# Kernel tuning notes

Measured on AMD Instinct MI355X. Metric: run time of the kernel, lower is better.

## Reference

```python
import jax, jax.numpy as jnp
import numpy as np

N = 100000      # nodes
E = 1600000     # edges (before self-loops)
IN_DIM = 128
HEADS1, C1 = 8, 16   # conv1: hidden_dim=16, heads=8 -> 128 concat
OUT_DIM = 40
NEG_SLOPE = 0.2


def setup_inputs() -> dict:
    key = jax.random.key(0)
    ks = jax.random.split(key, 10)
    s = 0.1
    x = jax.random.normal(ks[0], (N, IN_DIM), dtype=jnp.float32)
    edge_index = jax.random.randint(ks[1], (2, E), 0, N)
    W1 = jax.random.normal(ks[2], (IN_DIM, HEADS1 * C1), dtype=jnp.float32) * s
    att_l1 = jax.random.normal(ks[3], (HEADS1, C1), dtype=jnp.float32) * s
    att_r1 = jax.random.normal(ks[4], (HEADS1, C1), dtype=jnp.float32) * s
    b1 = jnp.zeros((HEADS1 * C1,), dtype=jnp.float32)
    W2 = jax.random.normal(ks[5], (HEADS1 * C1, OUT_DIM), dtype=jnp.float32) * s
    att_l2 = jax.random.normal(ks[6], (1, OUT_DIM), dtype=jnp.float32) * s
    att_r2 = jax.random.normal(ks[7], (1, OUT_DIM), dtype=jnp.float32) * s
    b2 = jnp.zeros((OUT_DIM,), dtype=jnp.float32)
    return {"x": x, "edge_index": edge_index, "W1": W1, "att_l1": att_l1,
            "att_r1": att_r1, "b1": b1, "W2": W2, "att_l2": att_l2,
            "att_r2": att_r2, "b2": b2}


def supergat_layer(x, src, dst, W, att_l, att_r, bias, concat):
    """One SuperGATConv layer, MX attention, inference mode (no dropout)."""
    n = x.shape[0]
    heads, out_ch = att_l.shape
    h = (x @ W).reshape(n, heads, out_ch)      # [N, H, C]
    h_i = h[dst]                               # target features  [E2, H, C]
    h_j = h[src]                               # source features  [E2, H, C]
    # MX attention: mix of GO (learned att vectors) gated by DP (dot product)
    logits = jnp.sum(h_i * h_j, axis=-1)                           # [E2, H]
    alpha = jnp.sum(h_j * att_l, axis=-1) + jnp.sum(h_i * att_r, axis=-1)
    alpha = alpha * jax.nn.sigmoid(logits)
    alpha = jax.nn.leaky_relu(alpha, NEG_SLOPE)
    # segment softmax over destination node (every node has a self-loop)
    a_max = jax.ops.segment_max(alpha, dst, num_segments=n)        # [N, H]
    ex = jnp.exp(alpha - a_max[dst])
    denom = jax.ops.segment_sum(ex, dst, num_segments=n)           # [N, H]
    a = ex / denom[dst]                                            # [E2, H]
    out = jax.ops.segment_sum(h_j * a[..., None], dst, num_segments=n)  # [N,H,C]
    if concat:
        out = out.reshape(n, heads * out_ch)
    else:
        out = out.mean(axis=1)
    return out + bias


def reference(x, edge_index, W1, att_l1, att_r1, b1, W2, att_l2, att_r2, b2):
    n = x.shape[0]
    loops = jnp.arange(n, dtype=edge_index.dtype)
    ei = jnp.concatenate([edge_index, jnp.stack([loops, loops])], axis=1)
    src, dst = ei[0], ei[1]
    h = supergat_layer(x, src, dst, W1, att_l1, att_r1, b1, concat=True)
    h = jax.nn.elu(h)
    out = supergat_layer(h, src, dst, W2, att_l2, att_r2, b2, concat=False)
    return jax.nn.log_softmax(out, axis=1)
```

## Files before the change

kernel.cpp:

```cpp
#include <hip/hip_runtime.h>
#include <math.h>

#define N_NODES 100000
#define N_EDGES 1600000
#define E2 (N_EDGES + N_NODES)
#define NEG_SLOPE 0.2f

#define NPB 128
#define NB  ((N_NODES + NPB - 1) / NPB)
#define CAP 2600
#define CAPP (CAP + 3 * NPB)
#define BSLACK (3 * NPB + 4)
#define BCH 4096

typedef unsigned int uint;
typedef unsigned short ushort;
typedef __attribute__((ext_vector_type(2))) _Float16 h2_t;
typedef __attribute__((ext_vector_type(8))) _Float16 f16x8;
typedef __attribute__((ext_vector_type(4))) float f32x4;

union U8 { uint4 q; f16x8 v; h2_t h2[4]; _Float16 h[8]; uint u[4]; };


__device__ inline ushort f2h(float x) {
  _Float16 h = (_Float16)x;
  return *(ushort*)&h;
}

__device__ inline float h2f(ushort u) {
  _Float16 h = *(_Float16*)&u;
  return (float)h;
}

__device__ inline h2_t pk2h(float a, float b) {
  auto r = __builtin_amdgcn_cvt_pkrtz(a, b);
  return *(h2_t*)&r;
}

__device__ inline float fdot2(h2_t a, h2_t b, float c) {
#if __has_builtin(__builtin_amdgcn_fdot2)
  return __builtin_amdgcn_fdot2(*(__fp16 __attribute__((ext_vector_type(2)))*)&a,
                                *(__fp16 __attribute__((ext_vector_type(2)))*)&b,
                                c, false);
#else
  return c + (float)a.x * (float)b.x + (float)a.y * (float)b.y;
#endif
}


__global__ __launch_bounds__(256) void k_prepW(const float* __restrict__ W1,
                                               const float* __restrict__ W2,
                                               ushort* __restrict__ WT1,
                                               ushort* __restrict__ WT2,
                                               int* __restrict__ bcursor) {
  int b = blockIdx.x, t = threadIdx.x;
  if (b == 0) {
    for (int i = t; i < 128 * 128; i += 256) {
      int k = i >> 7, n = i & 127;
      WT1[n * 128 + k] = f2h(W1[i]);
    }
  } else if (b == 1) {
    for (int i = t; i < 48 * 128; i += 256) {
      int n = i >> 7, k = i & 127;
      WT2[i] = (n < 40) ? f2h(W2[k * 40 + n]) : (ushort)0;
    }
  } else {
    for (int i = t; i < NB; i += 256) bcursor[i] = i * CAP;
  }
}


__global__ __launch_bounds__(256) void k_bucket(const int* __restrict__ ei,
                                                int* __restrict__ bcursor,
                                                uint* __restrict__ pbuf) {
  __shared__ uint pay[BCH];
  __shared__ ushort bkt[BCH];
  __shared__ int cnt[NB];
  __shared__ int base[NB];
  const int tid = threadIdx.x;
  const int ebase = blockIdx.x * BCH;
  for (int t = tid; t < NB; t += 256) cnt[t] = 0;
  __syncthreads();
#pragma unroll 4
  for (int k = 0; k < BCH / 256; ++k) {
    int idx = tid + k * 256;
    int e = ebase + idx;
    if (e < E2) {
      int s, d;
      if (e < N_EDGES) { s = ei[e]; d = ei[N_EDGES + e]; }
      else { s = e - N_EDGES; d = s; }
      pay[idx] = ((uint)s << 7) | (uint)(d & 127);
      int b = d >> 7;
      bkt[idx] = (ushort)b;
      atomicAdd(&cnt[b], 1);
    } else {
      bkt[idx] = 0xFFFFu;
    }
  }
  __syncthreads();
  for (int t = tid; t < NB; t += 256) {
    int c = cnt[t];
    base[t] = c ? atomicAdd(&bcursor[t], c) : 0;
    cnt[t] = 0;
  }
  __syncthreads();
#pragma unroll 4
  for (int k = 0; k < BCH / 256; ++k) {
    int idx = tid + k * 256;
    ushort b = bkt[idx];
    if (b != 0xFFFFu) {
      int pos = base[b] + atomicAdd(&cnt[b], 1);
      pbuf[pos] = pay[idx];
    }
  }
}

__global__ __launch_bounds__(1024) void k_scanB(const int* __restrict__ bcursor,
                                                int* __restrict__ bbase) {
  __shared__ int sm[1024];
  int t = threadIdx.x;
  int v = (t < NB) ? (bcursor[t] - t * CAP) : 0;
  sm[t] = v;
  __syncthreads();
  for (int off = 1; off < 1024; off <<= 1) {
    int u = (t >= off) ? sm[t - off] : 0;
    __syncthreads();
    sm[t] += u;
    __syncthreads();
  }
  if (t < NB) {
    int excl = sm[t] - v;
    bbase[t] = ((excl + 3) & ~3) + t * BSLACK;
  }
}

__global__ __launch_bounds__(128) void k_csr(const uint* __restrict__ pbuf,
                                             const int* __restrict__ bcursor,
                                             const int* __restrict__ bbase,
                                             int* __restrict__ rs,
                                             int* __restrict__ re,
                                             int* __restrict__ csr) {
  __shared__ int hist[NPB];
  __shared__ int excl[NPB];
  __shared__ int cur[NPB];
  __shared__ int lcsr[CAPP];
  const int b = blockIdx.x;
  const int tid = threadIdx.x;
  int count = bcursor[b] - b * CAP;
  if (count > CAP) count = CAP;
  const int gbase = bbase[b];
  const uint* seg = pbuf + b * CAP;
  hist[tid] = 0;
  __syncthreads();
  for (int k = tid; k < count; k += 128) atomicAdd(&hist[seg[k] & 127u], 1);
  __syncthreads();
  int rounded = (hist[tid] + 3) & ~3;
  excl[tid] = rounded;
  __syncthreads();
  for (int off = 1; off < 128; off <<= 1) {
    int u = (tid >= off) ? excl[tid - off] : 0;
    __syncthreads();
    excl[tid] += u;
    __syncthreads();
  }
  int ex = excl[tid] - rounded;
  cur[tid] = ex;
  int node = b * NPB + tid;
  if (node < N_NODES) {
    rs[node] = gbase + ex;
    re[node] = gbase + ex + rounded;
  }
  __syncthreads();
  const int ptotal = excl[NPB - 1];
  for (int k = tid; k < ptotal; k += 128) lcsr[k] = N_NODES;
  __syncthreads();
  for (int k = tid; k < count; k += 128) {
    uint pk = seg[k];
    int nd = pk & 127u;
    int pos = atomicAdd(&cur[nd], 1);
    lcsr[pos] = (int)(pk >> 7);
  }
  __syncthreads();
  for (int k = tid; k < ptotal; k += 128) csr[gbase + k] = lcsr[k];
}


__global__ __launch_bounds__(256) void k_gemm1m(const float* __restrict__ x,
                                                const ushort* __restrict__ WT1,
                                                const float* __restrict__ attl,
                                                const float* __restrict__ attr,
                                                ushort* __restrict__ h1h,
                                                ushort* __restrict__ al1h,
                                                float* __restrict__ ar1) {
  __shared__ ushort stg[4][16][136];
  __shared__ h2_t attl_sm[64], attr_sm[64];
  const int tid = threadIdx.x;
  const int w = tid >> 6, l = tid & 63;
  const int r16 = l & 15, kq = l >> 4;
  const int rowbase = blockIdx.x * 64 + w * 16;
  if (tid < 64) attl_sm[tid] = pk2h(attl[2 * tid], attl[2 * tid + 1]);
  else if (tid < 128) { int t = tid - 64; attr_sm[t] = pk2h(attr[2 * t], attr[2 * t + 1]); }
  if (blockIdx.x == 0) {
    if (tid >= 128 && tid < 144) ((uint4*)h1h)[(size_t)N_NODES * 16 + (tid - 128)] = make_uint4(0, 0, 0, 0);
    else if (tid >= 144 && tid < 152) al1h[(size_t)N_NODES * 8 + (tid - 144)] = (ushort)0xFC00;
  }
  int arow = rowbase + r16;
  if (arow > N_NODES - 1) arow = N_NODES - 1;
  f16x8 af[4];
  const float* xr = x + (size_t)arow * 128 + kq * 8;
#pragma unroll
  for (int t = 0; t < 4; ++t) {
    float4 a0 = *(const float4*)(xr + t * 32);
    float4 a1 = *(const float4*)(xr + t * 32 + 4);
    U8 u;
    u.h2[0] = pk2h(a0.x, a0.y); u.h2[1] = pk2h(a0.z, a0.w);
    u.h2[2] = pk2h(a1.x, a1.y); u.h2[3] = pk2h(a1.z, a1.w);
    af[t] = u.v;
  }
  f32x4 acc[8];
#pragma unroll
  for (int n = 0; n < 8; ++n) acc[n] = (f32x4){0.f, 0.f, 0.f, 0.f};
  const uint4* WT4 = (const uint4*)WT1;
#pragma unroll
  for (int t = 0; t < 4; ++t) {
#pragma unroll
    for (int n = 0; n < 8; ++n) {
      U8 b;
      b.q = WT4[(size_t)(n * 16 + r16) * 16 + t * 4 + kq];
      acc[n] = __builtin_amdgcn_mfma_f32_16x16x32_f16(af[t], b.v, acc[n], 0, 0, 0);
    }
  }
#pragma unroll
  for (int n = 0; n < 8; ++n) {
#pragma unroll
    for (int r = 0; r < 4; ++r) stg[w][kq * 4 + r][n * 16 + r16] = f2h(acc[n][r]);
  }
  __syncthreads();
  uint4* H1 = (uint4*)h1h;
  const uint4* S = (const uint4*)stg[w];
#pragma unroll
  for (int q = 0; q < 4; ++q) {
    int idx = l + q * 64;
    int row = idx >> 4, c4 = idx & 15;
    int grow = rowbase + row;
    if (grow < N_NODES) H1[(size_t)grow * 16 + c4] = S[row * 17 + c4];
  }
#pragma unroll
  for (int p = 0; p < 2; ++p) {
    int pidx = l + p * 64;
    int row = pidx >> 3, h = pidx & 7;
    int grow = rowbase + row;
    U8 a0, a1;
    a0.q = S[row * 17 + h * 2];
    a1.q = S[row * 17 + h * 2 + 1];
    float sl = 0.f, sr = 0.f;
#pragma unroll
    for (int k = 0; k < 4; ++k) {
      sl = fdot2(a0.h2[k], attl_sm[h * 8 + k], sl);
      sr = fdot2(a0.h2[k], attr_sm[h * 8 + k], sr);
      sl = fdot2(a1.h2[k], attl_sm[h * 8 + 4 + k], sl);
      sr = fdot2(a1.h2[k], attr_sm[h * 8 + 4 + k], sr);
    }
    if (grow < N_NODES) {
      al1h[(size_t)grow * 8 + h] = f2h(sl);
      ar1[(size_t)grow * 8 + h] = sr;
    }
  }
}


__global__ __launch_bounds__(256) void k_edge1(const ushort* __restrict__ h1h,
                                               const ushort* __restrict__ alT,
                                               const float* __restrict__ ar1,
                                               const int* __restrict__ rs,
                                               const int* __restrict__ re,
                                               const int* __restrict__ csr,
                                               const float* __restrict__ b1,
                                               ushort* __restrict__ y1h) {
  const int tid = threadIdx.x;
  const int lane = tid & 63;
  const int wv = tid >> 6;
  const int grp = lane >> 4;
  const int l = lane & 15;
  const int h = l >> 1;
  const int node0 = (blockIdx.x * 4 + wv) * 4 + grp;
  const bool alive = node0 < N_NODES;
  const int i = alive ? node0 : N_NODES - 1;
  const int start = rs[i], end = re[i];
  const char* Hb = (const char*)h1h;
  const char* Ab = (const char*)alT;
  const char* Cb = (const char*)csr;
  const uint loff = (uint)l * 16u;
  const uint aoff = (uint)h * 2u;
  U8 uhi;
  uhi.q = *(const uint4*)(Hb + (uint)i * 256u + loff);
  const float ar_i = ar1[i * 8 + h];
  float s = 0.f;
  f16x8 acc = {};
  int4 ja = *(const int4*)(Cb + (uint)start * 4u);
  for (int e = start; e < end; e += 4) {
    int ep = (e + 4 < end) ? e + 4 : e;
    int4 jn = *(const int4*)(Cb + (uint)ep * 4u);
    U8 u0, u1, u2, u3;
    u0.q = *(const uint4*)(Hb + (uint)ja.x * 256u + loff);
    u1.q = *(const uint4*)(Hb + (uint)ja.y * 256u + loff);
    u2.q = *(const uint4*)(Hb + (uint)ja.z * 256u + loff);
    u3.q = *(const uint4*)(Hb + (uint)ja.w * 256u + loff);
    float av0 = h2f(*(const ushort*)(Ab + (uint)ja.x * 16u + aoff));
    float av1 = h2f(*(const ushort*)(Ab + (uint)ja.y * 16u + aoff));
    float av2 = h2f(*(const ushort*)(Ab + (uint)ja.z * 16u + aoff));
    float av3 = h2f(*(const ushort*)(Ab + (uint)ja.w * 16u + aoff));
    float p0 = 0.f, p1 = 0.f, p2 = 0.f, p3 = 0.f;
#pragma unroll
    for (int k = 0; k < 4; ++k) {
      p0 = fdot2(uhi.h2[k], u0.h2[k], p0);
      p1 = fdot2(uhi.h2[k], u1.h2[k], p1);
      p2 = fdot2(uhi.h2[k], u2.h2[k], p2);
      p3 = fdot2(uhi.h2[k], u3.h2[k], p3);
    }
    p0 += __shfl_xor(p0, 1);
    p1 += __shfl_xor(p1, 1);
    p2 += __shfl_xor(p2, 1);
    p3 += __shfl_xor(p3, 1);
    float a0 = (av0 + ar_i) * (1.f / (1.f + __expf(-p0)));
    float a1 = (av1 + ar_i) * (1.f / (1.f + __expf(-p1)));
    float a2 = (av2 + ar_i) * (1.f / (1.f + __expf(-p2)));
    float a3 = (av3 + ar_i) * (1.f / (1.f + __expf(-p3)));
    a0 = fmaxf(a0, NEG_SLOPE * a0);
    a1 = fmaxf(a1, NEG_SLOPE * a1);
    a2 = fmaxf(a2, NEG_SLOPE * a2);
    a3 = fmaxf(a3, NEG_SLOPE * a3);
    float ex0 = __expf(a0);
    float ex1 = __expf(a1);
    float ex2 = __expf(a2);
    float ex3 = __expf(a3);
    s += (ex0 + ex1) + (ex2 + ex3);
    acc += u0.v * (_Float16)ex0;
    acc += u1.v * (_Float16)ex1;
    acc += u2.v * (_Float16)ex2;
    acc += u3.v * (_Float16)ex3;
    ja = jn;
  }
  float inv = 1.f / s;
  float4 bb0 = *(const float4*)(b1 + l * 8);
  float4 bb1 = *(const float4*)(b1 + l * 8 + 4);
  float o[8];
#pragma unroll
  for (int c = 0; c < 8; ++c) {
    float b = (c < 4) ? ((const float*)&bb0)[c] : ((const float*)&bb1)[c - 4];
    float v = (float)acc[c] * inv + b;
    o[c] = v > 0.f ? v : __expf(v) - 1.f;
  }
  if (alive) {
    U8 pk;
#pragma unroll
    for (int c = 0; c < 4; ++c) pk.h2[c] = pk2h(o[2 * c], o[2 * c + 1]);
    ((uint4*)y1h)[(size_t)i * 16 + l] = pk.q;
  }
}


__global__ __launch_bounds__(256) void k_gemm2m(const ushort* __restrict__ y1h,
                                                const ushort* __restrict__ WT2,
                                                const float* __restrict__ attl,
                                                const float* __restrict__ attr,
                                                ushort* __restrict__ h2p,
                                                float* __restrict__ al2,
                                                float* __restrict__ ar2) {
  __shared__ ushort stg[4][16][56];
  __shared__ h2_t attl_sm[20], attr_sm[20];
  const int tid = threadIdx.x;
  const int w = tid >> 6, l = tid & 63;
  const int r16 = l & 15, kq = l >> 4;
  const int rowbase = blockIdx.x * 64 + w * 16;
  if (tid < 20) attl_sm[tid] = pk2h(attl[2 * tid], attl[2 * tid + 1]);
  else if (tid >= 32 && tid < 52) { int t = tid - 32; attr_sm[t] = pk2h(attr[2 * t], attr[2 * t + 1]); }
  if (blockIdx.x == 0) {
    if (tid >= 64 && tid < 69) ((uint4*)h2p)[(size_t)N_NODES * 5 + (tid - 64)] = make_uint4(0, 0, 0, 0);
    else if (tid == 69) al2[N_NODES] = -INFINITY;
  }
  int arow = rowbase + r16;
  if (arow > N_NODES - 1) arow = N_NODES - 1;
  const uint4* Y4 = (const uint4*)y1h;
  f16x8 af[4];
#pragma unroll
  for (int t = 0; t < 4; ++t) {
    U8 u;
    u.q = Y4[(size_t)arow * 16 + t * 4 + kq];
    af[t] = u.v;
  }
  f32x4 acc[3];
#pragma unroll
  for (int n = 0; n < 3; ++n) acc[n] = (f32x4){0.f, 0.f, 0.f, 0.f};
  const uint4* WT4 = (const uint4*)WT2;
#pragma unroll
  for (int t = 0; t < 4; ++t) {
#pragma unroll
    for (int n = 0; n < 3; ++n) {
      U8 b;
      b.q = WT4[(size_t)(n * 16 + r16) * 16 + t * 4 + kq];
      acc[n] = __builtin_amdgcn_mfma_f32_16x16x32_f16(af[t], b.v, acc[n], 0, 0, 0);
    }
  }
#pragma unroll
  for (int n = 0; n < 3; ++n) {
#pragma unroll
    for (int r = 0; r < 4; ++r) stg[w][kq * 4 + r][n * 16 + r16] = f2h(acc[n][r]);
  }
  __syncthreads();
  uint4* H2 = (uint4*)h2p;
  const uint4* S = (const uint4*)stg[w];
#pragma unroll
  for (int q = 0; q < 2; ++q) {
    int idx = l + q * 64;
    if (idx < 80) {
      int row = idx / 5, c4 = idx % 5;
      int grow = rowbase + row;
      if (grow < N_NODES) H2[(size_t)grow * 5 + c4] = S[row * 7 + c4];
    }
  }
  if (l < 32) {
    int row = l & 15, sel = l >> 4;
    int grow = rowbase + row;
    const h2_t* att = sel ? attr_sm : attl_sm;
    float v = 0.f;
#pragma unroll
    for (int q = 0; q < 5; ++q) {
      U8 b;
      b.q = S[row * 7 + q];
#pragma unroll
      for (int k = 0; k < 4; ++k) v = fdot2(b.h2[k], att[q * 4 + k], v);
    }
    if (grow < N_NODES) {
      if (sel) ar2[grow] = v;
      else     al2[grow] = v;
    }
  }
}


__global__ __launch_bounds__(256) void k_edge2(const ushort* __restrict__ h2p,
                                               const float* __restrict__ alT,
                                               const float* __restrict__ ar2,
                                               const int* __restrict__ rs,
                                               const int* __restrict__ re,
                                               const int* __restrict__ csr,
                                               const float* __restrict__ b2,
                                               float* __restrict__ out) {
  const int tid = threadIdx.x;
  const int lane = tid & 63;
  const int wv = tid >> 6;
  const int grp = lane >> 3;
  const int l = lane & 7;
  const int node0 = (blockIdx.x * 4 + wv) * 8 + grp;
  const bool alive = node0 < N_NODES;
  const int i = alive ? node0 : N_NODES - 1;
  const int start = rs[i], end = re[i];
  const char* Hb = (const char*)h2p;
  const char* Cb = (const char*)csr;
  const uint loff = (uint)(l < 5 ? l : 0) * 16u;
  U8 uhi;
  uhi.q = *(const uint4*)(Hb + (uint)i * 80u + loff);
  if (l >= 5) uhi.q = make_uint4(0, 0, 0, 0);
  const float ar_i = ar2[i];
  float s = 0.f;
  f16x8 acc = {};
  int4 ja = *(const int4*)(Cb + (uint)start * 4u);
  for (int e = start; e < end; e += 4) {
    int ep = (e + 4 < end) ? e + 4 : e;
    int4 jn = *(const int4*)(Cb + (uint)ep * 4u);
    U8 u0, u1, u2, u3;
    u0.q = *(const uint4*)(Hb + (uint)ja.x * 80u + loff);
    u1.q = *(const uint4*)(Hb + (uint)ja.y * 80u + loff);
    u2.q = *(const uint4*)(Hb + (uint)ja.z * 80u + loff);
    u3.q = *(const uint4*)(Hb + (uint)ja.w * 80u + loff);
    float av0 = alT[ja.x], av1 = alT[ja.y], av2 = alT[ja.z], av3 = alT[ja.w];
    float p0 = 0.f, p1 = 0.f, p2 = 0.f, p3 = 0.f;
#pragma unroll
    for (int k = 0; k < 4; ++k) {
      p0 = fdot2(uhi.h2[k], u0.h2[k], p0);
      p1 = fdot2(uhi.h2[k], u1.h2[k], p1);
      p2 = fdot2(uhi.h2[k], u2.h2[k], p2);
      p3 = fdot2(uhi.h2[k], u3.h2[k], p3);
    }
#pragma unroll
    for (int m = 1; m <= 4; m <<= 1) {
      p0 += __shfl_xor(p0, m);
      p1 += __shfl_xor(p1, m);
      p2 += __shfl_xor(p2, m);
      p3 += __shfl_xor(p3, m);
    }
    float a0 = (av0 + ar_i) * (1.f / (1.f + __expf(-p0)));
    float a1 = (av1 + ar_i) * (1.f / (1.f + __expf(-p1)));
    float a2 = (av2 + ar_i) * (1.f / (1.f + __expf(-p2)));
    float a3 = (av3 + ar_i) * (1.f / (1.f + __expf(-p3)));
    a0 = fmaxf(a0, NEG_SLOPE * a0);
    a1 = fmaxf(a1, NEG_SLOPE * a1);
    a2 = fmaxf(a2, NEG_SLOPE * a2);
    a3 = fmaxf(a3, NEG_SLOPE * a3);
    float ex0 = __expf(a0);
    float ex1 = __expf(a1);
    float ex2 = __expf(a2);
    float ex3 = __expf(a3);
    s += (ex0 + ex1) + (ex2 + ex3);
    acc += u0.v * (_Float16)ex0;
    acc += u1.v * (_Float16)ex1;
    acc += u2.v * (_Float16)ex2;
    acc += u3.v * (_Float16)ex3;
    ja = jn;
  }
  float inv = 1.f / s;
  bool act = l < 5;
  float o[8];
  float mx = -1e30f;
#pragma unroll
  for (int c = 0; c < 8; ++c) {
    float b = act ? b2[l * 8 + c] : 0.f;
    o[c] = (float)acc[c] * inv + b;
    if (act) mx = fmaxf(mx, o[c]);
  }
  mx = fmaxf(mx, __shfl_xor(mx, 1));
  mx = fmaxf(mx, __shfl_xor(mx, 2));
  mx = fmaxf(mx, __shfl_xor(mx, 4));
  float se = 0.f;
  if (act) {
#pragma unroll
    for (int c = 0; c < 8; ++c) se += __expf(o[c] - mx);
  }
  se += __shfl_xor(se, 1);
  se += __shfl_xor(se, 2);
  se += __shfl_xor(se, 4);
  if (alive && act) {
    float lse = mx + __logf(se);
    float4 r0 = make_float4(o[0] - lse, o[1] - lse, o[2] - lse, o[3] - lse);
    float4 r1 = make_float4(o[4] - lse, o[5] - lse, o[6] - lse, o[7] - lse);
    float4* O = (float4*)(out + (size_t)i * 40 + l * 8);
    O[0] = r0;
    O[1] = r1;
  }
}


extern "C" void kernel_launch(void* const* d_in, const int* in_sizes, int n_in,
                              void* d_out, int out_size, void* d_ws, size_t ws_size,
                              hipStream_t stream) {
  const float* x     = (const float*)d_in[0];
  const int*   ei    = (const int*)d_in[1];
  const float* W1    = (const float*)d_in[2];
  const float* attl1 = (const float*)d_in[3];
  const float* attr1 = (const float*)d_in[4];
  const float* b1    = (const float*)d_in[5];
  const float* W2    = (const float*)d_in[6];
  const float* attl2 = (const float*)d_in[7];
  const float* attr2 = (const float*)d_in[8];
  const float* b2    = (const float*)d_in[9];
  float* out = (float*)d_out;

  char* wsp = (char*)d_ws;
  size_t off = 0;
  auto alloc = [&](size_t bytes) {
    char* p = wsp + off;
    off = (off + bytes + 255) & ~(size_t)255;
    return p;
  };
  ushort* h1h   = (ushort*)alloc((size_t)(N_NODES + 1) * 128 * 2);
  ushort* y1h   = (ushort*)alloc((size_t)N_NODES * 128 * 2);
  ushort* al1h  = (ushort*)alloc((size_t)(N_NODES + 1) * 8 * 2);
  float* ar1    = (float*)alloc((size_t)N_NODES * 8 * 4);
  int* rs       = (int*)alloc((size_t)(N_NODES + 4) * 4);
  int* re       = (int*)alloc((size_t)(N_NODES + 4) * 4);
  int* bcursor  = (int*)alloc((size_t)NB * 4);
  int* bbase    = (int*)alloc((size_t)NB * 4);
  int* csr      = (int*)alloc((size_t)(E2 + NB * BSLACK + 16) * 4);
  ushort* WT1   = (ushort*)alloc(128 * 128 * 2);
  ushort* WT2   = (ushort*)alloc(48 * 128 * 2);
  uint* pbuf  = (uint*)y1h;
  ushort* h2p = h1h;
  float* al2  = (float*)ar1;
  float* ar2  = al2 + N_NODES + 8;

  k_prepW<<<3, 256, 0, stream>>>(W1, W2, WT1, WT2, bcursor);
  k_bucket<<<(E2 + BCH - 1) / BCH, 256, 0, stream>>>(ei, bcursor, pbuf);
  k_scanB<<<1, 1024, 0, stream>>>(bcursor, bbase);
  k_csr<<<NB, 128, 0, stream>>>(pbuf, bcursor, bbase, rs, re, csr);

  k_gemm1m<<<(N_NODES + 63) / 64, 256, 0, stream>>>(x, WT1, attl1, attr1, h1h, al1h, ar1);
  k_edge1<<<(N_NODES + 15) / 16, 256, 0, stream>>>(h1h, al1h, ar1, rs, re, csr, b1, y1h);

  k_gemm2m<<<(N_NODES + 63) / 64, 256, 0, stream>>>(y1h, WT2, attl2, attr2, h2p, al2, ar2);
  k_edge2<<<(N_NODES + 31) / 32, 256, 0, stream>>>(h2p, al2, ar2, rs, re, csr, b2, out);
}
```

Before: 232.7 us.

## Recompute layer-1 source attention in edge loop; pack layer-2 al into h2 rows

Layer 1 no longer stores a per-node al1 array. The edge kernel now recomputes the source attention term with extra fdot2 ops against a half-precision copy of att_l, which removes one scattered 2-byte gather per edge. Padding edges (index N_NODES) are masked explicitly, since the sentinel al value is gone. Layer 2 widens each h2 row from 80 to 96 bytes and stores al2 (truncated to bf16-like precision) in the spare slot, where it is read back with a shuffle instead of a separate gather. The cost is more arithmetic per edge in layer 1, more bytes gathered per edge in layer 2, and a small loss of precision in al2.

```diff
diff --git a/kernel.cpp b/kernel.cpp
--- a/kernel.cpp
+++ b/kernel.cpp
@@ -50,8 +50,10 @@
 
 __global__ __launch_bounds__(256) void k_prepW(const float* __restrict__ W1,
                                                const float* __restrict__ W2,
+                                               const float* __restrict__ attl1,
                                                ushort* __restrict__ WT1,
                                                ushort* __restrict__ WT2,
+                                               ushort* __restrict__ attl1h,
                                                int* __restrict__ bcursor) {
   int b = blockIdx.x, t = threadIdx.x;
   if (b == 0) {
@@ -64,6 +66,7 @@
       int n = i >> 7, k = i & 127;
       WT2[i] = (n < 40) ? f2h(W2[k * 40 + n]) : (ushort)0;
     }
+    if (t < 128) attl1h[t] = f2h(attl1[t]);
   } else {
     for (int i = t; i < NB; i += 256) bcursor[i] = i * CAP;
   }
@@ -187,22 +190,18 @@
 
 __global__ __launch_bounds__(256) void k_gemm1m(const float* __restrict__ x,
                                                 const ushort* __restrict__ WT1,
-                                                const float* __restrict__ attl,
                                                 const float* __restrict__ attr,
                                                 ushort* __restrict__ h1h,
-                                                ushort* __restrict__ al1h,
                                                 float* __restrict__ ar1) {
   __shared__ ushort stg[4][16][136];
-  __shared__ h2_t attl_sm[64], attr_sm[64];
+  __shared__ h2_t attr_sm[64];
   const int tid = threadIdx.x;
   const int w = tid >> 6, l = tid & 63;
   const int r16 = l & 15, kq = l >> 4;
   const int rowbase = blockIdx.x * 64 + w * 16;
-  if (tid < 64) attl_sm[tid] = pk2h(attl[2 * tid], attl[2 * tid + 1]);
-  else if (tid < 128) { int t = tid - 64; attr_sm[t] = pk2h(attr[2 * t], attr[2 * t + 1]); }
+  if (tid < 64) attr_sm[tid] = pk2h(attr[2 * tid], attr[2 * tid + 1]);
   if (blockIdx.x == 0) {
     if (tid >= 128 && tid < 144) ((uint4*)h1h)[(size_t)N_NODES * 16 + (tid - 128)] = make_uint4(0, 0, 0, 0);
-    else if (tid >= 144 && tid < 152) al1h[(size_t)N_NODES * 8 + (tid - 144)] = (ushort)0xFC00;
   }
   int arow = rowbase + r16;
   if (arow > N_NODES - 1) arow = N_NODES - 1;
@@ -253,24 +252,19 @@
     U8 a0, a1;
     a0.q = S[row * 17 + h * 2];
     a1.q = S[row * 17 + h * 2 + 1];
-    float sl = 0.f, sr = 0.f;
+    float sr = 0.f;
 #pragma unroll
     for (int k = 0; k < 4; ++k) {
-      sl = fdot2(a0.h2[k], attl_sm[h * 8 + k], sl);
       sr = fdot2(a0.h2[k], attr_sm[h * 8 + k], sr);
-      sl = fdot2(a1.h2[k], attl_sm[h * 8 + 4 + k], sl);
       sr = fdot2(a1.h2[k], attr_sm[h * 8 + 4 + k], sr);
     }
-    if (grow < N_NODES) {
-      al1h[(size_t)grow * 8 + h] = f2h(sl);
-      ar1[(size_t)grow * 8 + h] = sr;
-    }
+    if (grow < N_NODES) ar1[(size_t)grow * 8 + h] = sr;
   }
 }
 
 
 __global__ __launch_bounds__(256) void k_edge1(const ushort* __restrict__ h1h,
-                                               const ushort* __restrict__ alT,
+                                               const ushort* __restrict__ attl1h,
                                                const float* __restrict__ ar1,
                                                const int* __restrict__ rs,
                                                const int* __restrict__ re,
@@ -288,12 +282,11 @@
   const int i = alive ? node0 : N_NODES - 1;
   const int start = rs[i], end = re[i];
   const char* Hb = (const char*)h1h;
-  const char* Ab = (const char*)alT;
   const char* Cb = (const char*)csr;
   const uint loff = (uint)l * 16u;
-  const uint aoff = (uint)h * 2u;
-  U8 uhi;
+  U8 uhi, au;
   uhi.q = *(const uint4*)(Hb + (uint)i * 256u + loff);
+  au.q = *(const uint4*)(attl1h + l * 8);
   const float ar_i = ar1[i * 8 + h];
   float s = 0.f;
   f16x8 acc = {};
@@ -306,22 +299,197 @@
     u1.q = *(const uint4*)(Hb + (uint)ja.y * 256u + loff);
     u2.q = *(const uint4*)(Hb + (uint)ja.z * 256u + loff);
     u3.q = *(const uint4*)(Hb + (uint)ja.w * 256u + loff);
-    float av0 = h2f(*(const ushort*)(Ab + (uint)ja.x * 16u + aoff));
-    float av1 = h2f(*(const ushort*)(Ab + (uint)ja.y * 16u + aoff));
-    float av2 = h2f(*(const ushort*)(Ab + (uint)ja.z * 16u + aoff));
-    float av3 = h2f(*(const ushort*)(Ab + (uint)ja.w * 16u + aoff));
     float p0 = 0.f, p1 = 0.f, p2 = 0.f, p3 = 0.f;
+    float q0 = 0.f, q1 = 0.f, q2 = 0.f, q3 = 0.f;
 #pragma unroll
     for (int k = 0; k < 4; ++k) {
       p0 = fdot2(uhi.h2[k], u0.h2[k], p0);
       p1 = fdot2(uhi.h2[k], u1.h2[k], p1);
       p2 = fdot2(uhi.h2[k], u2.h2[k], p2);
       p3 = fdot2(uhi.h2[k], u3.h2[k], p3);
-    }
-    p0 += __shfl_xor(p0, 1);
-    p1 += __shfl_xor(p1, 1);
-    p2 += __shfl_xor(p2, 1);
-    p3 += __shfl_xor(p3, 1);
+      q0 = fdot2(au.h2[k], u0.h2[k], q0);
+      q1 = fdot2(au.h2[k], u1.h2[k], q1);
+      q2 = fdot2(au.h2[k], u2.h2[k], q2);
+      q3 = fdot2(au.h2[k], u3.h2[k], q3);
+    }
+    p0 += __shfl_xor(p0, 1); q0 += __shfl_xor(q0, 1);
+    p1 += __shfl_xor(p1, 1); q1 += __shfl_xor(q1, 1);
+    p2 += __shfl_xor(p2, 1); q2 += __shfl_xor(q2, 1);
+    p3 += __shfl_xor(p3, 1); q3 += __shfl_xor(q3, 1);
+    float a0 = (q0 + ar_i) * (1.f / (1.f + __expf(-p0)));
+    float a1 = (q1 + ar_i) * (1.f / (1.f + __expf(-p1)));
+    float a2 = (q2 + ar_i) * (1.f / (1.f + __expf(-p2)));
+    float a3 = (q3 + ar_i) * (1.f / (1.f + __expf(-p3)));
+    a0 = fmaxf(a0, NEG_SLOPE * a0);
+    a1 = fmaxf(a1, NEG_SLOPE * a1);
+    a2 = fmaxf(a2, NEG_SLOPE * a2);
+    a3 = fmaxf(a3, NEG_SLOPE * a3);
+    float ex0 = (ja.x != N_NODES) ? __expf(a0) : 0.f;
+    float ex1 = (ja.y != N_NODES) ? __expf(a1) : 0.f;
+    float ex2 = (ja.z != N_NODES) ? __expf(a2) : 0.f;
+    float ex3 = (ja.w != N_NODES) ? __expf(a3) : 0.f;
+    s += (ex0 + ex1) + (ex2 + ex3);
+    acc += u0.v * (_Float16)ex0;
+    acc += u1.v * (_Float16)ex1;
+    acc += u2.v * (_Float16)ex2;
+    acc += u3.v * (_Float16)ex3;
+    ja = jn;
+  }
+  float inv = 1.f / s;
+  float4 bb0 = *(const float4*)(b1 + l * 8);
+  float4 bb1 = *(const float4*)(b1 + l * 8 + 4);
+  float o[8];
+#pragma unroll
+  for (int c = 0; c < 8; ++c) {
+    float b = (c < 4) ? ((const float*)&bb0)[c] : ((const float*)&bb1)[c - 4];
+    float v = (float)acc[c] * inv + b;
+    o[c] = v > 0.f ? v : __expf(v) - 1.f;
+  }
+  if (alive) {
+    U8 pk;
+#pragma unroll
+    for (int c = 0; c < 4; ++c) pk.h2[c] = pk2h(o[2 * c], o[2 * c + 1]);
+    ((uint4*)y1h)[(size_t)i * 16 + l] = pk.q;
+  }
+}
+
+
+__global__ __launch_bounds__(256) void k_gemm2m(const ushort* __restrict__ y1h,
+                                                const ushort* __restrict__ WT2,
+                                                const float* __restrict__ attl,
+                                                const float* __restrict__ attr,
+                                                ushort* __restrict__ h2p,
+                                                float* __restrict__ ar2) {
+  __shared__ ushort stg[4][16][56];
+  __shared__ h2_t attl_sm[20], attr_sm[20];
+  const int tid = threadIdx.x;
+  const int w = tid >> 6, l = tid & 63;
+  const int r16 = l & 15, kq = l >> 4;
+  const int rowbase = blockIdx.x * 64 + w * 16;
+  if (tid < 20) attl_sm[tid] = pk2h(attl[2 * tid], attl[2 * tid + 1]);
+  else if (tid >= 32 && tid < 52) { int t = tid - 32; attr_sm[t] = pk2h(attr[2 * t], attr[2 * t + 1]); }
+  if (blockIdx.x == 0) {
+    if (tid >= 64 && tid < 70) {
+      int c = tid - 64;
+      uint4 v = make_uint4(0, 0, 0, 0);
+      if (c == 5) v.x = __float_as_uint(-1e30f) & 0xFFFF0000u;
+      ((uint4*)h2p)[(size_t)N_NODES * 6 + c] = v;
+    }
+  }
+  int arow = rowbase + r16;
+  if (arow > N_NODES - 1) arow = N_NODES - 1;
+  const uint4* Y4 = (const uint4*)y1h;
+  f16x8 af[4];
+#pragma unroll
+  for (int t = 0; t < 4; ++t) {
+    U8 u;
+    u.q = Y4[(size_t)arow * 16 + t * 4 + kq];
+    af[t] = u.v;
+  }
+  f32x4 acc[3];
+#pragma unroll
+  for (int n = 0; n < 3; ++n) acc[n] = (f32x4){0.f, 0.f, 0.f, 0.f};
+  const uint4* WT4 = (const uint4*)WT2;
+#pragma unroll
+  for (int t = 0; t < 4; ++t) {
+#pragma unroll
+    for (int n = 0; n < 3; ++n) {
+      U8 b;
+      b.q = WT4[(size_t)(n * 16 + r16) * 16 + t * 4 + kq];
+      acc[n] = __builtin_amdgcn_mfma_f32_16x16x32_f16(af[t], b.v, acc[n], 0, 0, 0);
+    }
+  }
+#pragma unroll
+  for (int n = 0; n < 3; ++n) {
+#pragma unroll
+    for (int r = 0; r < 4; ++r) stg[w][kq * 4 + r][n * 16 + r16] = f2h(acc[n][r]);
+  }
+  __syncthreads();
+  uint4* H2 = (uint4*)h2p;
+  const uint4* S = (const uint4*)stg[w];
+#pragma unroll
+  for (int q = 0; q < 2; ++q) {
+    int idx = l + q * 64;
+    if (idx < 80) {
+      int row = idx / 5, c4 = idx % 5;
+      int grow = rowbase + row;
+      if (grow < N_NODES) H2[(size_t)grow * 6 + c4] = S[row * 7 + c4];
+    }
+  }
+  if (l < 32) {
+    int row = l & 15, sel = l >> 4;
+    int grow = rowbase + row;
+    const h2_t* att = sel ? attr_sm : attl_sm;
+    float v = 0.f;
+#pragma unroll
+    for (int q = 0; q < 5; ++q) {
+      U8 b;
+      b.q = S[row * 7 + q];
+#pragma unroll
+      for (int k = 0; k < 4; ++k) v = fdot2(b.h2[k], att[q * 4 + k], v);
+    }
+    if (grow < N_NODES) {
+      if (sel) ar2[grow] = v;
+      else     H2[(size_t)grow * 6 + 5] = make_uint4(__float_as_uint(v) & 0xFFFF0000u, 0, 0, 0);
+    }
+  }
+}
+
+
+__global__ __launch_bounds__(256) void k_edge2(const ushort* __restrict__ h2p,
+                                               const float* __restrict__ ar2,
+                                               const int* __restrict__ rs,
+                                               const int* __restrict__ re,
+                                               const int* __restrict__ csr,
+                                               const float* __restrict__ b2,
+                                               float* __restrict__ out) {
+  const int tid = threadIdx.x;
+  const int lane = tid & 63;
+  const int wv = tid >> 6;
+  const int grp = lane >> 3;
+  const int l = lane & 7;
+  const int node0 = (blockIdx.x * 4 + wv) * 8 + grp;
+  const bool alive = node0 < N_NODES;
+  const int i = alive ? node0 : N_NODES - 1;
+  const int start = rs[i], end = re[i];
+  const char* Hb = (const char*)h2p;
+  const char* Cb = (const char*)csr;
+  const uint loff = (uint)(l <= 5 ? l : 0) * 16u;
+  const int srcl = (lane & 56) | 5;
+  U8 uhi;
+  uhi.q = *(const uint4*)(Hb + (uint)i * 96u + loff);
+  if (l >= 5) uhi.q = make_uint4(0, 0, 0, 0);
+  const float ar_i = ar2[i];
+  float s = 0.f;
+  f16x8 acc = {};
+  int4 ja = *(const int4*)(Cb + (uint)start * 4u);
+  for (int e = start; e < end; e += 4) {
+    int ep = (e + 4 < end) ? e + 4 : e;
+    int4 jn = *(const int4*)(Cb + (uint)ep * 4u);
+    U8 u0, u1, u2, u3;
+    u0.q = *(const uint4*)(Hb + (uint)ja.x * 96u + loff);
+    u1.q = *(const uint4*)(Hb + (uint)ja.y * 96u + loff);
+    u2.q = *(const uint4*)(Hb + (uint)ja.z * 96u + loff);
+    u3.q = *(const uint4*)(Hb + (uint)ja.w * 96u + loff);
+    float av0 = __uint_as_float((uint)__shfl((int)u0.u[0], srcl));
+    float av1 = __uint_as_float((uint)__shfl((int)u1.u[0], srcl));
+    float av2 = __uint_as_float((uint)__shfl((int)u2.u[0], srcl));
+    float av3 = __uint_as_float((uint)__shfl((int)u3.u[0], srcl));
+    float p0 = 0.f, p1 = 0.f, p2 = 0.f, p3 = 0.f;
+#pragma unroll
+    for (int k = 0; k < 4; ++k) {
+      p0 = fdot2(uhi.h2[k], u0.h2[k], p0);
+      p1 = fdot2(uhi.h2[k], u1.h2[k], p1);
+      p2 = fdot2(uhi.h2[k], u2.h2[k], p2);
+      p3 = fdot2(uhi.h2[k], u3.h2[k], p3);
+    }
+#pragma unroll
+    for (int m = 1; m <= 4; m <<= 1) {
+      p0 += __shfl_xor(p0, m);
+      p1 += __shfl_xor(p1, m);
+      p2 += __shfl_xor(p2, m);
+      p3 += __shfl_xor(p3, m);
+    }
     float a0 = (av0 + ar_i) * (1.f / (1.f + __expf(-p0)));
     float a1 = (av1 + ar_i) * (1.f / (1.f + __expf(-p1)));
     float a2 = (av2 + ar_i) * (1.f / (1.f + __expf(-p2)));
@@ -342,174 +510,6 @@
     ja = jn;
   }
   float inv = 1.f / s;
-  float4 bb0 = *(const float4*)(b1 + l * 8);
-  float4 bb1 = *(const float4*)(b1 + l * 8 + 4);
-  float o[8];
-#pragma unroll
-  for (int c = 0; c < 8; ++c) {
-    float b = (c < 4) ? ((const float*)&bb0)[c] : ((const float*)&bb1)[c - 4];
-    float v = (float)acc[c] * inv + b;
-    o[c] = v > 0.f ? v : __expf(v) - 1.f;
-  }
-  if (alive) {
-    U8 pk;
-#pragma unroll
-    for (int c = 0; c < 4; ++c) pk.h2[c] = pk2h(o[2 * c], o[2 * c + 1]);
-    ((uint4*)y1h)[(size_t)i * 16 + l] = pk.q;
-  }
-}
-
-
-__global__ __launch_bounds__(256) void k_gemm2m(const ushort* __restrict__ y1h,
-                                                const ushort* __restrict__ WT2,
-                                                const float* __restrict__ attl,
-                                                const float* __restrict__ attr,
-                                                ushort* __restrict__ h2p,
-                                                float* __restrict__ al2,
-                                                float* __restrict__ ar2) {
-  __shared__ ushort stg[4][16][56];
-  __shared__ h2_t attl_sm[20], attr_sm[20];
-  const int tid = threadIdx.x;
-  const int w = tid >> 6, l = tid & 63;
-  const int r16 = l & 15, kq = l >> 4;
-  const int rowbase = blockIdx.x * 64 + w * 16;
-  if (tid < 20) attl_sm[tid] = pk2h(attl[2 * tid], attl[2 * tid + 1]);
-  else if (tid >= 32 && tid < 52) { int t = tid - 32; attr_sm[t] = pk2h(attr[2 * t], attr[2 * t + 1]); }
-  if (blockIdx.x == 0) {
-    if (tid >= 64 && tid < 69) ((uint4*)h2p)[(size_t)N_NODES * 5 + (tid - 64)] = make_uint4(0, 0, 0, 0);
-    else if (tid == 69) al2[N_NODES] = -INFINITY;
-  }
-  int arow = rowbase + r16;
-  if (arow > N_NODES - 1) arow = N_NODES - 1;
-  const uint4* Y4 = (const uint4*)y1h;
-  f16x8 af[4];
-#pragma unroll
-  for (int t = 0; t < 4; ++t) {
-    U8 u;
-    u.q = Y4[(size_t)arow * 16 + t * 4 + kq];
-    af[t] = u.v;
-  }
-  f32x4 acc[3];
-#pragma unroll
-  for (int n = 0; n < 3; ++n) acc[n] = (f32x4){0.f, 0.f, 0.f, 0.f};
-  const uint4* WT4 = (const uint4*)WT2;
-#pragma unroll
-  for (int t = 0; t < 4; ++t) {
-#pragma unroll
-    for (int n = 0; n < 3; ++n) {
-      U8 b;
-      b.q = WT4[(size_t)(n * 16 + r16) * 16 + t * 4 + kq];
-      acc[n] = __builtin_amdgcn_mfma_f32_16x16x32_f16(af[t], b.v, acc[n], 0, 0, 0);
-    }
-  }
-#pragma unroll
-  for (int n = 0; n < 3; ++n) {
-#pragma unroll
-    for (int r = 0; r < 4; ++r) stg[w][kq * 4 + r][n * 16 + r16] = f2h(acc[n][r]);
-  }
-  __syncthreads();
-  uint4* H2 = (uint4*)h2p;
-  const uint4* S = (const uint4*)stg[w];
-#pragma unroll
-  for (int q = 0; q < 2; ++q) {
-    int idx = l + q * 64;
-    if (idx < 80) {
-      int row = idx / 5, c4 = idx % 5;
-      int grow = rowbase + row;
-      if (grow < N_NODES) H2[(size_t)grow * 5 + c4] = S[row * 7 + c4];
-    }
-  }
-  if (l < 32) {
-    int row = l & 15, sel = l >> 4;
-    int grow = rowbase + row;
-    const h2_t* att = sel ? attr_sm : attl_sm;
-    float v = 0.f;
-#pragma unroll
-    for (int q = 0; q < 5; ++q) {
-      U8 b;
-      b.q = S[row * 7 + q];
-#pragma unroll
-      for (int k = 0; k < 4; ++k) v = fdot2(b.h2[k], att[q * 4 + k], v);
-    }
-    if (grow < N_NODES) {
-      if (sel) ar2[grow] = v;
-      else     al2[grow] = v;
-    }
-  }
-}
-
-
-__global__ __launch_bounds__(256) void k_edge2(const ushort* __restrict__ h2p,
-                                               const float* __restrict__ alT,
-                                               const float* __restrict__ ar2,
-                                               const int* __restrict__ rs,
-                                               const int* __restrict__ re,
-                                               const int* __restrict__ csr,
-                                               const float* __restrict__ b2,
-                                               float* __restrict__ out) {
-  const int tid = threadIdx.x;
-  const int lane = tid & 63;
-  const int wv = tid >> 6;
-  const int grp = lane >> 3;
-  const int l = lane & 7;
-  const int node0 = (blockIdx.x * 4 + wv) * 8 + grp;
-  const bool alive = node0 < N_NODES;
-  const int i = alive ? node0 : N_NODES - 1;
-  const int start = rs[i], end = re[i];
-  const char* Hb = (const char*)h2p;
-  const char* Cb = (const char*)csr;
-  const uint loff = (uint)(l < 5 ? l : 0) * 16u;
-  U8 uhi;
-  uhi.q = *(const uint4*)(Hb + (uint)i * 80u + loff);
-  if (l >= 5) uhi.q = make_uint4(0, 0, 0, 0);
-  const float ar_i = ar2[i];
-  float s = 0.f;
-  f16x8 acc = {};
-  int4 ja = *(const int4*)(Cb + (uint)start * 4u);
-  for (int e = start; e < end; e += 4) {
-    int ep = (e + 4 < end) ? e + 4 : e;
-    int4 jn = *(const int4*)(Cb + (uint)ep * 4u);
-    U8 u0, u1, u2, u3;
-    u0.q = *(const uint4*)(Hb + (uint)ja.x * 80u + loff);
-    u1.q = *(const uint4*)(Hb + (uint)ja.y * 80u + loff);
-    u2.q = *(const uint4*)(Hb + (uint)ja.z * 80u + loff);
-    u3.q = *(const uint4*)(Hb + (uint)ja.w * 80u + loff);
-    float av0 = alT[ja.x], av1 = alT[ja.y], av2 = alT[ja.z], av3 = alT[ja.w];
-    float p0 = 0.f, p1 = 0.f, p2 = 0.f, p3 = 0.f;
-#pragma unroll
-    for (int k = 0; k < 4; ++k) {
-      p0 = fdot2(uhi.h2[k], u0.h2[k], p0);
-      p1 = fdot2(uhi.h2[k], u1.h2[k], p1);
-      p2 = fdot2(uhi.h2[k], u2.h2[k], p2);
-      p3 = fdot2(uhi.h2[k], u3.h2[k], p3);
-    }
-#pragma unroll
-    for (int m = 1; m <= 4; m <<= 1) {
-      p0 += __shfl_xor(p0, m);
-      p1 += __shfl_xor(p1, m);
-      p2 += __shfl_xor(p2, m);
-      p3 += __shfl_xor(p3, m);
-    }
-    float a0 = (av0 + ar_i) * (1.f / (1.f + __expf(-p0)));
-    float a1 = (av1 + ar_i) * (1.f / (1.f + __expf(-p1)));
-    float a2 = (av2 + ar_i) * (1.f / (1.f + __expf(-p2)));
-    float a3 = (av3 + ar_i) * (1.f / (1.f + __expf(-p3)));
-    a0 = fmaxf(a0, NEG_SLOPE * a0);
-    a1 = fmaxf(a1, NEG_SLOPE * a1);
-    a2 = fmaxf(a2, NEG_SLOPE * a2);
-    a3 = fmaxf(a3, NEG_SLOPE * a3);
-    float ex0 = __expf(a0);
-    float ex1 = __expf(a1);
-    float ex2 = __expf(a2);
-    float ex3 = __expf(a3);
-    s += (ex0 + ex1) + (ex2 + ex3);
-    acc += u0.v * (_Float16)ex0;
-    acc += u1.v * (_Float16)ex1;
-    acc += u2.v * (_Float16)ex2;
-    acc += u3.v * (_Float16)ex3;
-    ja = jn;
-  }
-  float inv = 1.f / s;
   bool act = l < 5;
   float o[8];
   float mx = -1e30f;
@@ -565,7 +565,6 @@
   };
   ushort* h1h   = (ushort*)alloc((size_t)(N_NODES + 1) * 128 * 2);
   ushort* y1h   = (ushort*)alloc((size_t)N_NODES * 128 * 2);
-  ushort* al1h  = (ushort*)alloc((size_t)(N_NODES + 1) * 8 * 2);
   float* ar1    = (float*)alloc((size_t)N_NODES * 8 * 4);
   int* rs       = (int*)alloc((size_t)(N_NODES + 4) * 4);
   int* re       = (int*)alloc((size_t)(N_NODES + 4) * 4);
@@ -574,19 +573,19 @@
   int* csr      = (int*)alloc((size_t)(E2 + NB * BSLACK + 16) * 4);
   ushort* WT1   = (ushort*)alloc(128 * 128 * 2);
   ushort* WT2   = (ushort*)alloc(48 * 128 * 2);
+  ushort* attl1h = (ushort*)alloc(128 * 2);
   uint* pbuf  = (uint*)y1h;
   ushort* h2p = h1h;
-  float* al2  = (float*)ar1;
-  float* ar2  = al2 + N_NODES + 8;
-
-  k_prepW<<<3, 256, 0, stream>>>(W1, W2, WT1, WT2, bcursor);
+  float* ar2  = (float*)ar1;
+
+  k_prepW<<<3, 256, 0, stream>>>(W1, W2, attl1, WT1, WT2, attl1h, bcursor);
   k_bucket<<<(E2 + BCH - 1) / BCH, 256, 0, stream>>>(ei, bcursor, pbuf);
   k_scanB<<<1, 1024, 0, stream>>>(bcursor, bbase);
   k_csr<<<NB, 128, 0, stream>>>(pbuf, bcursor, bbase, rs, re, csr);
 
-  k_gemm1m<<<(N_NODES + 63) / 64, 256, 0, stream>>>(x, WT1, attl1, attr1, h1h, al1h, ar1);
-  k_edge1<<<(N_NODES + 15) / 16, 256, 0, stream>>>(h1h, al1h, ar1, rs, re, csr, b1, y1h);
-
-  k_gemm2m<<<(N_NODES + 63) / 64, 256, 0, stream>>>(y1h, WT2, attl2, attr2, h2p, al2, ar2);
-  k_edge2<<<(N_NODES + 31) / 32, 256, 0, stream>>>(h2p, al2, ar2, rs, re, csr, b2, out);
-}
+  k_gemm1m<<<(N_NODES + 63) / 64, 256, 0, stream>>>(x, WT1, attr1, h1h, ar1);
+  k_edge1<<<(N_NODES + 15) / 16, 256, 0, stream>>>(h1h, attl1h, ar1, rs, re, csr, b1, y1h);
+
+  k_gemm2m<<<(N_NODES + 63) / 64, 256, 0, stream>>>(y1h, WT2, attl2, attr2, h2p, ar2);
+  k_edge2<<<(N_NODES + 31) / 32, 256, 0, stream>>>(h2p, ar2, rs, re, csr, b2, out);
+}
```

New measurement: 218.9 us. 1.06x faster.
